# Performance work log

Hardware: AMD Instinct MI355X
Metric: run time of the kernel (lower is better)

## Reference

```python
import jax, jax.numpy as jnp
import numpy as np

D_MODEL = 1024
N_HEADS = 16
D_K = D_MODEL // N_HEADS
SEQ = 4096
BATCH = 1
THETA = 10000.0


def setup_inputs() -> dict:
    key = jax.random.key(0)
    ks = jax.random.split(key, 5)
    scale = 0.02
    x = jax.random.normal(ks[0], (BATCH, SEQ, D_MODEL), dtype=jnp.float32)
    token_positions = jnp.broadcast_to(jnp.arange(SEQ, dtype=jnp.int64 if jax.config.jax_enable_x64 else jnp.int32)[None, :], (BATCH, SEQ))
    Wq = jax.random.normal(ks[1], (D_MODEL, D_MODEL), dtype=jnp.float32) * scale
    Wk = jax.random.normal(ks[2], (D_MODEL, D_MODEL), dtype=jnp.float32) * scale
    Wv = jax.random.normal(ks[3], (D_MODEL, D_MODEL), dtype=jnp.float32) * scale
    Wo = jax.random.normal(ks[4], (D_MODEL, D_MODEL), dtype=jnp.float32) * scale
    return {"x": x, "token_positions": token_positions, "Wq": Wq, "Wk": Wk, "Wv": Wv, "Wo": Wo}


def _apply_rope(t, token_positions, theta=THETA):
    # t: (b, h, s, d_k); token_positions: (b, s)
    d_k = t.shape[-1]
    inv_freq = theta ** (-jnp.arange(0, d_k, 2, dtype=jnp.float32) / d_k)  # (d_k/2,)
    ang = token_positions.astype(jnp.float32)[:, :, None] * inv_freq  # (b, s, d_k/2)
    cos = jnp.cos(ang)[:, None, :, :]  # (b, 1, s, d_k/2)
    sin = jnp.sin(ang)[:, None, :, :]
    te, to = t[..., 0::2], t[..., 1::2]
    re = te * cos - to * sin
    ro = te * sin + to * cos
    # interleave back: (..., d_k/2, 2) -> (..., d_k)
    return jnp.stack([re, ro], axis=-1).reshape(t.shape)


def reference(x, token_positions, Wq, Wk, Wv, Wo):
    b, s, d_model = x.shape
    h, d_k = N_HEADS, D_K
    q = (x @ Wq.T).reshape(b, s, h, d_k).transpose(0, 2, 1, 3)  # (b,h,s,d_k)
    k = (x @ Wk.T).reshape(b, s, h, d_k).transpose(0, 2, 1, 3)
    v = (x @ Wv.T).reshape(b, s, h, d_k).transpose(0, 2, 1, 3)
    q = _apply_rope(q, token_positions)
    k = _apply_rope(k, token_positions)
    scores = jnp.einsum('bhqd,bhkd->bhqk', q, k) / jnp.sqrt(jnp.float32(d_k))
    causal = jnp.tril(jnp.ones((s, s), dtype=bool))[None, None]
    scores = jnp.where(causal, scores, jnp.float32(-1e9))
    attn = jax.nn.softmax(scores, axis=-1)
    out = jnp.einsum('bhqk,bhkd->bhqd', attn, v)  # (b,h,s,d_k)
    out = out.transpose(0, 2, 1, 3).reshape(b, s, d_model)
    return out @ Wo.T
```

## Files before the change

kernel.cpp:

```cpp
#include <hip/hip_runtime.h>
#include <hip/hip_bf16.h>
#include <math.h>


#define SEQ 4096
#define DM  1024
#define NH  16
#define DK  64

typedef __attribute__((ext_vector_type(8))) short short8;
typedef __attribute__((ext_vector_type(4))) float floatx4;
typedef __attribute__((ext_vector_type(16))) float floatx16;
typedef __attribute__((ext_vector_type(4))) short short4v;

static __device__ __forceinline__ short f2bf(float f) {
    __hip_bfloat16 h = __float2bfloat16(f);
    return __builtin_bit_cast(short, h);
}

static __device__ __forceinline__ float fast_exp2(float x) {
#if __has_builtin(__builtin_amdgcn_exp2f)
    return __builtin_amdgcn_exp2f(x);
#else
    return exp2f(x);
#endif
}

static __device__ __forceinline__ short8 load8_f32_as_bf16(const float* p) {
    float4 a = *reinterpret_cast<const float4*>(p);
    float4 b = *reinterpret_cast<const float4*>(p + 4);
    short8 s;
    s[0] = f2bf(a.x); s[1] = f2bf(a.y); s[2] = f2bf(a.z); s[3] = f2bf(a.w);
    s[4] = f2bf(b.x); s[5] = f2bf(b.y); s[6] = f2bf(b.z); s[7] = f2bf(b.w);
    return s;
}

static __device__ __forceinline__ void gl2lds16(const __hip_bfloat16* g, short* l) {
    __builtin_amdgcn_global_load_lds(
        (const __attribute__((address_space(1))) unsigned int*)g,
        (__attribute__((address_space(3))) unsigned int*)l, 16, 0, 0);
}

static __device__ __forceinline__ int read_pos(const int* tp32, int s) {
    return (tp32[1] == 1) ? tp32[s] : tp32[2 * s];
}

__global__ __launch_bounds__(256) void prep_kernel(
    const float* __restrict__ x,  const float* __restrict__ Wq,
    const float* __restrict__ Wk, const float* __restrict__ Wv,
    const int* __restrict__ tp,
    __hip_bfloat16* __restrict__ xb,  __hip_bfloat16* __restrict__ Wqb,
    __hip_bfloat16* __restrict__ Wkb, __hip_bfloat16* __restrict__ Wvb,
    float2* __restrict__ tab)
{
    int b = blockIdx.x;
    if (b < 3584) {
        const float* src; __hip_bfloat16* dst; int off;
        if (b < 2048)      { src = x;  dst = xb;  off = b; }
        else if (b < 2560) { src = Wq; dst = Wqb; off = b - 2048; }
        else if (b < 3072) { src = Wk; dst = Wkb; off = b - 2560; }
        else               { src = Wv; dst = Wvb; off = b - 3072; }
        size_t i = (size_t)off * 256 + threadIdx.x;
        short8 v = load8_f32_as_bf16(src + i * 8);
        *reinterpret_cast<short8*>((short*)dst + i * 8) = v;
    } else {
        int idx = (b - 3584) * 256 + threadIdx.x;
        if (idx < SEQ * 32) {
            int s = idx >> 5, pair = idx & 31;
            float inv_freq = exp2f(-(float)(2 * pair) * (13.287712379549449f / 64.f));
            float sn, cs;
            sincosf((float)read_pos(tp, s) * inv_freq, &sn, &cs);
            tab[idx] = make_float2(cs, sn);
        }
    }
}

__global__ __launch_bounds__(256) void qkv_rope_kernel(
    const __hip_bfloat16* __restrict__ xb,
    const float2* __restrict__ tab,
    const __hip_bfloat16* __restrict__ Wqb,
    const __hip_bfloat16* __restrict__ Wkb,
    const __hip_bfloat16* __restrict__ Wvb,
    __hip_bfloat16* __restrict__ q_ws,
    __hip_bfloat16* __restrict__ k_ws,
    __hip_bfloat16* __restrict__ vt_ws)
{
    __shared__ __align__(16) short pool[17408];
    short* As = pool;
    short* Bs = pool + 8192;

    const int by = blockIdx.y;
    const int wsel = by >> 3;
    const __hip_bfloat16* W = (wsel == 0) ? Wqb : (wsel == 1 ? Wkb : Wvb);
    const int nloc0 = (by & 7) * 128;
    const int m0 = blockIdx.x * 128;

    const int t = threadIdx.x;
    const int lane = t & 63;
    const int w = t >> 6;
    const int quad = lane >> 4;
    const int ln = lane & 15;
    const int wm = (w >> 1) * 64;
    const int wn = (w & 1) * 64;

    floatx4 acc[4][4];
    #pragma unroll
    for (int i = 0; i < 4; i++)
        #pragma unroll
        for (int j = 0; j < 4; j++) acc[i][j] = (floatx4){0.f, 0.f, 0.f, 0.f};

    for (int k0 = 0; k0 < DM; k0 += 64) {
        #pragma unroll
        for (int it = 0; it < 4; it++) {
            int row = w * 32 + it * 8 + (lane >> 3);
            int sg = (lane & 7) ^ (row & 7);
            gl2lds16(&xb[(size_t)(m0 + row) * DM + k0 + sg * 8], &As[(w * 32 + it * 8) * 64]);
            gl2lds16(&W[(size_t)(nloc0 + row) * DM + k0 + sg * 8], &Bs[(w * 32 + it * 8) * 64]);
        }
        __syncthreads();

        short8 af[4][2], bfr[4][2];
        #pragma unroll
        for (int i = 0; i < 4; i++)
            #pragma unroll
            for (int kc = 0; kc < 2; kc++)
                af[i][kc] = *reinterpret_cast<const short8*>(
                    &As[(wm + i * 16 + ln) * 64 + (((kc * 4 + quad) ^ (ln & 7)) << 3)]);
        #pragma unroll
        for (int j = 0; j < 4; j++)
            #pragma unroll
            for (int kc = 0; kc < 2; kc++)
                bfr[j][kc] = *reinterpret_cast<const short8*>(
                    &Bs[(wn + j * 16 + ln) * 64 + (((kc * 4 + quad) ^ (ln & 7)) << 3)]);

        #pragma unroll
        for (int kc = 0; kc < 2; kc++)
            #pragma unroll
            for (int i = 0; i < 4; i++)
                #pragma unroll
                for (int j = 0; j < 4; j++)
                    acc[i][j] = __builtin_amdgcn_mfma_f32_16x16x32_bf16(
                        af[i][kc], bfr[j][kc], acc[i][j], 0, 0, 0);
        __syncthreads();
    }

    if (wsel < 2) {
        __hip_bfloat16* dst = (wsel == 0) ? q_ws : k_ws;
        const float qscale = (wsel == 0) ? 0.18033688011112042f : 1.0f;
        #pragma unroll
        for (int j = 0; j < 4; j++) {
            int cnl = wn + j * 16 + ln;
            int pair = ((nloc0 + cnl) & 63) >> 1;
            #pragma unroll
            for (int i = 0; i < 4; i++) {
                int rowl = wm + i * 16 + quad * 4;
                #pragma unroll
                for (int r = 0; r < 4; r++) {
                    float2 t2 = tab[(size_t)(m0 + rowl + r) * 32 + pair];
                    float val = acc[i][j][r];
                    float partner = __shfl_xor(val, 1, 64);
                    float res = val * t2.x + (((lane & 1) ? partner : -partner) * t2.y);
                    pool[(rowl + r) * 136 + cnl] = f2bf(res * qscale);
                }
            }
        }
        __syncthreads();
        int row = t >> 1, half = t & 1;
        size_t gbase = (size_t)(m0 + row) * DM + nloc0 + half * 64;
        #pragma unroll
        for (int c = 0; c < 8; c++)
            *reinterpret_cast<short8*>(&dst[gbase + c * 8]) =
                *reinterpret_cast<const short8*>(&pool[row * 136 + half * 64 + c * 8]);
    } else {
        #pragma unroll
        for (int j = 0; j < 4; j++) {
            int cnl = wn + j * 16 + ln;
            #pragma unroll
            for (int i = 0; i < 4; i++) {
                int s0 = wm + i * 16 + quad * 4;
                #pragma unroll
                for (int r = 0; r < 4; r++)
                    pool[cnl * 136 + s0 + r] = f2bf(acc[i][j][r]);
            }
        }
        __syncthreads();
        int cnl = t >> 1, sh = t & 1;
        size_t base = (size_t)(nloc0 + cnl) * SEQ + m0 + sh * 64;
        #pragma unroll
        for (int c = 0; c < 8; c++)
            *reinterpret_cast<short8*>(&vt_ws[base + c * 8]) =
                *reinterpret_cast<const short8*>(&pool[cnl * 136 + sh * 64 + c * 8]);
    }
}

__global__ __launch_bounds__(1024, 1) void attn_kernel(
    const __hip_bfloat16* __restrict__ q_ws,
    const __hip_bfloat16* __restrict__ k_ws,
    const __hip_bfloat16* __restrict__ vt_ws,
    __hip_bfloat16* __restrict__ o_ws)
{
    __shared__ __align__(16) short Kt[2][128 * 64];
    __shared__ __align__(16) short Vt[2][64 * 128];

    const int bid = (int)blockIdx.x;
    const int head = bid & 15;
    const int jp = bid >> 4;

    const int t = threadIdx.x;
    const int lane = t & 63;
    const int w = t >> 6;
    const int ww = w & 3;
    const int kq = w >> 2;
    const int hi = lane >> 5;
    const int l31 = lane & 31;

    auto stage = [&](int b, int kb) {
        {
            int r = w * 8 + (lane >> 3);
            int keyloc = (r & ~12) | ((r & 4) << 1) | ((r & 8) >> 1);
            int g = (lane & 7) ^ (r & 7);
            gl2lds16(&k_ws[(size_t)(kb + keyloc) * DM + head * 64 + g * 8],
                     &Kt[b][(w * 8) * 64]);
        }
        {
            int d = w * 4 + (lane >> 4);
            int g = (lane & 15) ^ (d & 7);
            gl2lds16(&vt_ws[(size_t)(head * 64 + d) * SEQ + kb + g * 8],
                     &Vt[b][(w * 4) * 128]);
        }
    };

    #pragma unroll 1
    for (int pass = 0; pass < 2; pass++) {
        const int tile = pass ? jp : (31 - jp);
        const int nstep = tile + 1;
        const int q0 = tile * 128 + ww * 32;

        short8 qf[4];
        #pragma unroll
        for (int c = 0; c < 4; c++)
            qf[c] = *reinterpret_cast<const short8*>(
                &q_ws[(size_t)(q0 + l31) * DM + head * 64 + c * 16 + hi * 8]);

        floatx16 accO[2];
        #pragma unroll
        for (int db = 0; db < 2; db++)
            #pragma unroll
            for (int i = 0; i < 16; i++) accO[db][i] = 0.f;
        float l = 0.f;

        __syncthreads();
        stage(0, 0);
        int buf = 0;
        for (int st = 0; st < nstep; st++) {
            __syncthreads();
            if (st + 1 < nstep) stage(buf ^ 1, (st + 1) * 128);
            const bool last = (st == nstep - 1);

            if (!(last && kq > ww)) {
                const int kb32 = kq;
                const int krow = kb32 * 32 + l31;
                short8 kfr[4];
                #pragma unroll
                for (int kc = 0; kc < 4; kc++) {
                    int g = (kc * 2 + hi) ^ (krow & 7);
                    kfr[kc] = *reinterpret_cast<const short8*>(&Kt[buf][krow * 64 + g * 8]);
                }
                floatx16 s;
                #pragma unroll
                for (int i = 0; i < 16; i++) s[i] = 0.f;
                __builtin_amdgcn_s_setprio(1);
                #pragma unroll
                for (int kc = 0; kc < 4; kc++)
                    s = __builtin_amdgcn_mfma_f32_32x32x16_bf16(kfr[kc], qf[kc], s, 0, 0, 0);
                __builtin_amdgcn_s_setprio(0);

                if (last) {
                    #pragma unroll
                    for (int r = 0; r < 16; r++) {
                        int key_l = kb32 * 32 + (r & 7) + 2 * (r & 8) + 8 * hi;
                        if (key_l > ww * 32 + l31) s[r] = -1e9f;
                    }
                }
                float p[16];
                #pragma unroll
                for (int r = 0; r < 16; r++) { p[r] = fast_exp2(s[r]); l += p[r]; }

                union { short8 v; short e[8]; } pb[2];
                #pragma unroll
                for (int c = 0; c < 2; c++)
                    #pragma unroll
                    for (int e8 = 0; e8 < 8; e8++)
                        pb[c].e[e8] = f2bf(p[c * 8 + e8]);

                #pragma unroll
                for (int db = 0; db < 2; db++) {
                    const int vrow = db * 32 + l31;
                    short8 vfr[2];
                    #pragma unroll
                    for (int c = 0; c < 2; c++) {
                        int g = (kb32 * 4 + c * 2 + hi) ^ (vrow & 7);
                        vfr[c] = *reinterpret_cast<const short8*>(&Vt[buf][vrow * 128 + g * 8]);
                    }
                    __builtin_amdgcn_s_setprio(1);
                    accO[db] = __builtin_amdgcn_mfma_f32_32x32x16_bf16(vfr[0], pb[0].v, accO[db], 0, 0, 0);
                    accO[db] = __builtin_amdgcn_mfma_f32_32x32x16_bf16(vfr[1], pb[1].v, accO[db], 0, 0, 0);
                    __builtin_amdgcn_s_setprio(0);
                }
            }
            buf ^= 1;
        }

        float* scrK = (float*)Kt;
        float* scrV = (float*)Vt;
        __syncthreads();
        {
            const int slot = (ww * 2 + (kq & 1)) * 64 + lane;
            if (kq >= 2) {
                #pragma unroll
                for (int i = 0; i < 16; i++) scrK[i * 512 + slot] = accO[0][i];
                scrV[slot] = l;
            }
            __syncthreads();
            if (kq < 2) {
                #pragma unroll
                for (int i = 0; i < 16; i++) accO[0][i] += scrK[i * 512 + slot];
                l += scrV[slot];
            }
            __syncthreads();
            if (kq >= 2) {
                #pragma unroll
                for (int i = 0; i < 16; i++) scrK[i * 512 + slot] = accO[1][i];
            }
            __syncthreads();
            if (kq < 2) {
                #pragma unroll
                for (int i = 0; i < 16; i++) accO[1][i] += scrK[i * 512 + slot];
            }
            __syncthreads();
            const int slot2 = ww * 64 + lane;
            if (kq == 1) {
                #pragma unroll
                for (int i = 0; i < 16; i++) scrK[i * 256 + slot2] = accO[0][i];
                #pragma unroll
                for (int i = 0; i < 16; i++) scrK[(16 + i) * 256 + slot2] = accO[1][i];
                scrV[slot2] = l;
            }
            __syncthreads();
            if (kq == 0) {
                #pragma unroll
                for (int i = 0; i < 16; i++) accO[0][i] += scrK[i * 256 + slot2];
                #pragma unroll
                for (int i = 0; i < 16; i++) accO[1][i] += scrK[(16 + i) * 256 + slot2];
                l += scrV[slot2];
            }
        }

        float lf = l + __shfl_xor(l, 32, 64);
        float rl = 1.f / lf;

        __syncthreads();
        short* pool = (short*)Kt;
        if (kq == 0) {
            const int qrow = ww * 32 + l31;
            #pragma unroll
            for (int db = 0; db < 2; db++)
                #pragma unroll
                for (int j = 0; j < 4; j++) {
                    union { short4v v; short e[4]; } g;
                    #pragma unroll
                    for (int m = 0; m < 4; m++)
                        g.e[m] = f2bf(accO[db][j * 4 + m] * rl);
                    int dcol = db * 32 + j * 8 + 4 * hi;
                    *reinterpret_cast<short4v*>(&pool[qrow * 68 + dcol]) = g.v;
                }
        }
        __syncthreads();

        {
            int r = t >> 3, c8 = t & 7;
            size_t gb = (size_t)(tile * 128 + r) * DM + head * 64 + c8 * 8;
            union { short8 v8; short4v h[2]; } u;
            u.h[0] = *reinterpret_cast<const short4v*>(&pool[r * 68 + c8 * 8]);
            u.h[1] = *reinterpret_cast<const short4v*>(&pool[r * 68 + c8 * 8 + 4]);
            *reinterpret_cast<short8*>(&o_ws[gb]) = u.v8;
        }
    }
}

__global__ __launch_bounds__(256) void oproj_kernel(
    const __hip_bfloat16* __restrict__ o_in,
    const float* __restrict__ Wo,
    float* __restrict__ out)
{
    __shared__ __align__(16) char smem[24576];
    short* As = (short*)smem;
    short* Bs = As + 8192;
    float* fpool = (float*)smem;

    const int m0 = blockIdx.x * 128;
    const int n0 = blockIdx.y * 64;

    const int t = threadIdx.x;
    const int lane = t & 63;
    const int w = t >> 6;
    const int quad = lane >> 4;
    const int ln = lane & 15;
    const int wm = (w >> 1) * 64;
    const int wn = (w & 1) * 32;

    floatx4 acc[4][2];
    #pragma unroll
    for (int i = 0; i < 4; i++)
        #pragma unroll
        for (int j = 0; j < 2; j++) acc[i][j] = (floatx4){0.f, 0.f, 0.f, 0.f};

    for (int k0 = 0; k0 < DM; k0 += 64) {
        #pragma unroll
        for (int it = 0; it < 4; it++) {
            int row = w * 32 + it * 8 + (lane >> 3);
            int sg = (lane & 7) ^ (row & 7);
            gl2lds16(&o_in[(size_t)(m0 + row) * DM + k0 + sg * 8], &As[(w * 32 + it * 8) * 64]);
        }
        #pragma unroll
        for (int p = 0; p < 2; p++) {
            int r = (t >> 3) + p * 32;
            int sg2 = t & 7;
            *reinterpret_cast<short8*>(&Bs[r * 64 + ((sg2 ^ (r & 7)) << 3)]) =
                load8_f32_as_bf16(&Wo[(size_t)(n0 + r) * DM + k0 + sg2 * 8]);
        }
        __syncthreads();

        short8 af[4][2], bfr[2][2];
        #pragma unroll
        for (int i = 0; i < 4; i++)
            #pragma unroll
            for (int kc = 0; kc < 2; kc++)
                af[i][kc] = *reinterpret_cast<const short8*>(
                    &As[(wm + i * 16 + ln) * 64 + (((kc * 4 + quad) ^ (ln & 7)) << 3)]);
        #pragma unroll
        for (int j = 0; j < 2; j++)
            #pragma unroll
            for (int kc = 0; kc < 2; kc++)
                bfr[j][kc] = *reinterpret_cast<const short8*>(
                    &Bs[(wn + j * 16 + ln) * 64 + (((kc * 4 + quad) ^ (ln & 7)) << 3)]);

        #pragma unroll
        for (int kc = 0; kc < 2; kc++)
            #pragma unroll
            for (int i = 0; i < 4; i++)
                #pragma unroll
                for (int j = 0; j < 2; j++)
                    acc[i][j] = __builtin_amdgcn_mfma_f32_16x16x32_bf16(
                        af[i][kc], bfr[j][kc], acc[i][j], 0, 0, 0);
        __syncthreads();
    }

    #pragma unroll
    for (int ph = 0; ph < 2; ph++) {
        if ((w >> 1) == ph) {
            #pragma unroll
            for (int j = 0; j < 2; j++)
                #pragma unroll
                for (int i = 0; i < 4; i++) {
                    int rl = i * 16 + quad * 4;
                    #pragma unroll
                    for (int r = 0; r < 4; r++)
                        fpool[(rl + r) * 68 + wn + j * 16 + ln] = acc[i][j][r];
                }
        }
        __syncthreads();
        int row = t >> 2;
        int c0 = (t & 3) * 16;
        size_t gbase = (size_t)(m0 + ph * 64 + row) * DM + n0 + c0;
        #pragma unroll
        for (int c = 0; c < 4; c++)
            *reinterpret_cast<float4*>(&out[gbase + c * 4]) =
                *reinterpret_cast<const float4*>(&fpool[row * 68 + c0 + c * 4]);
        __syncthreads();
    }
}

extern "C" void kernel_launch(void* const* d_in, const int* in_sizes, int n_in,
                              void* d_out, int out_size, void* d_ws, size_t ws_size,
                              hipStream_t stream) {
    const float* x  = (const float*)d_in[0];
    const int* tp   = (const int*)d_in[1];
    const float* Wq = (const float*)d_in[2];
    const float* Wk = (const float*)d_in[3];
    const float* Wv = (const float*)d_in[4];
    const float* Wo = (const float*)d_in[5];
    float* out = (float*)d_out;

    char* ws = (char*)d_ws;
    const size_t MB = 1024 * 1024;
    __hip_bfloat16* xb    = (__hip_bfloat16*)(ws);
    __hip_bfloat16* q_ws  = (__hip_bfloat16*)(ws + 8  * MB);
    __hip_bfloat16* k_ws  = (__hip_bfloat16*)(ws + 16 * MB);
    __hip_bfloat16* vt_ws = (__hip_bfloat16*)(ws + 24 * MB);
    __hip_bfloat16* o_ws  = xb;
    __hip_bfloat16* Wqb = (__hip_bfloat16*)d_out;
    __hip_bfloat16* Wkb = Wqb + (size_t)DM * DM;
    __hip_bfloat16* Wvb = Wkb + (size_t)DM * DM;
    float2* tab = (float2*)((char*)d_out + 6 * MB);

    prep_kernel<<<4096, 256, 0, stream>>>(x, Wq, Wk, Wv, tp, xb, Wqb, Wkb, Wvb, tab);
    qkv_rope_kernel<<<dim3(32, 24), 256, 0, stream>>>(xb, tab, Wqb, Wkb, Wvb, q_ws, k_ws, vt_ws);
    attn_kernel<<<256, 1024, 0, stream>>>(q_ws, k_ws, vt_ws, o_ws);
    oproj_kernel<<<dim3(32, 16), 256, 0, stream>>>(o_ws, Wo, out);
}
```

Measured before the change: 205.0 us.

## Software-pipeline PV matmul one step behind QK in attention loop

Restructures the attention inner loop so the P·V MFMAs for the previous key tile run while the current tile's QK^T scores and exp are computed. V gains a third LDS buffer so the lagging tile stays resident, and a trailing P·V step is added after the loop. The setprio hints are dropped. The aim is to hide the softmax/exp latency behind matrix work and so remove the serial dependency between them. The cost is more LDS use and more live registers, which could hurt scheduling.

```diff
diff --git a/kernel.cpp b/kernel.cpp
--- a/kernel.cpp
+++ b/kernel.cpp
@@ -200,7 +200,7 @@
     __hip_bfloat16* __restrict__ o_ws)
 {
     __shared__ __align__(16) short Kt[2][128 * 64];
-    __shared__ __align__(16) short Vt[2][64 * 128];
+    __shared__ __align__(16) short Vt[3][64 * 128];
 
     const int bid = (int)blockIdx.x;
     const int head = bid & 15;
@@ -214,19 +214,19 @@
     const int hi = lane >> 5;
     const int l31 = lane & 31;
 
-    auto stage = [&](int b, int kb) {
+    auto stage = [&](int s, int kb) {
         {
             int r = w * 8 + (lane >> 3);
             int keyloc = (r & ~12) | ((r & 4) << 1) | ((r & 8) >> 1);
             int g = (lane & 7) ^ (r & 7);
             gl2lds16(&k_ws[(size_t)(kb + keyloc) * DM + head * 64 + g * 8],
-                     &Kt[b][(w * 8) * 64]);
+                     &Kt[s & 1][(w * 8) * 64]);
         }
         {
             int d = w * 4 + (lane >> 4);
             int g = (lane & 15) ^ (d & 7);
             gl2lds16(&vt_ws[(size_t)(head * 64 + d) * SEQ + kb + g * 8],
-                     &Vt[b][(w * 4) * 128]);
+                     &Vt[s % 3][(w * 4) * 128]);
         }
     };
 
@@ -248,37 +248,59 @@
             #pragma unroll
             for (int i = 0; i < 16; i++) accO[db][i] = 0.f;
         float l = 0.f;
+        short8 pbA, pbB;
 
         __syncthreads();
         stage(0, 0);
-        int buf = 0;
         for (int st = 0; st < nstep; st++) {
             __syncthreads();
-            if (st + 1 < nstep) stage(buf ^ 1, (st + 1) * 128);
+            if (st + 1 < nstep) stage(st + 1, (st + 1) * 128);
             const bool last = (st == nstep - 1);
-
-            if (!(last && kq > ww)) {
-                const int kb32 = kq;
-                const int krow = kb32 * 32 + l31;
-                short8 kfr[4];
+            const bool qk_act = !(last && kq > ww);
+
+            short8 kfr[4];
+            if (qk_act) {
+                const int krow = kq * 32 + l31;
                 #pragma unroll
                 for (int kc = 0; kc < 4; kc++) {
                     int g = (kc * 2 + hi) ^ (krow & 7);
-                    kfr[kc] = *reinterpret_cast<const short8*>(&Kt[buf][krow * 64 + g * 8]);
-                }
+                    kfr[kc] = *reinterpret_cast<const short8*>(&Kt[st & 1][krow * 64 + g * 8]);
+                }
+            }
+            short8 vfp[2][2];
+            if (st > 0) {
+                const short* Vp = Vt[(st - 1) % 3];
+                #pragma unroll
+                for (int db = 0; db < 2; db++) {
+                    const int vrow = db * 32 + l31;
+                    #pragma unroll
+                    for (int c = 0; c < 2; c++) {
+                        int g = (kq * 4 + c * 2 + hi) ^ (vrow & 7);
+                        vfp[db][c] = *reinterpret_cast<const short8*>(&Vp[vrow * 128 + g * 8]);
+                    }
+                }
+            }
+
+            if (st > 0) {
+                #pragma unroll
+                for (int db = 0; db < 2; db++) {
+                    accO[db] = __builtin_amdgcn_mfma_f32_32x32x16_bf16(vfp[db][0], pbA, accO[db], 0, 0, 0);
+                    accO[db] = __builtin_amdgcn_mfma_f32_32x32x16_bf16(vfp[db][1], pbB, accO[db], 0, 0, 0);
+                }
+            }
+
+            if (qk_act) {
                 floatx16 s;
                 #pragma unroll
                 for (int i = 0; i < 16; i++) s[i] = 0.f;
-                __builtin_amdgcn_s_setprio(1);
                 #pragma unroll
                 for (int kc = 0; kc < 4; kc++)
                     s = __builtin_amdgcn_mfma_f32_32x32x16_bf16(kfr[kc], qf[kc], s, 0, 0, 0);
-                __builtin_amdgcn_s_setprio(0);
 
                 if (last) {
                     #pragma unroll
                     for (int r = 0; r < 16; r++) {
-                        int key_l = kb32 * 32 + (r & 7) + 2 * (r & 8) + 8 * hi;
+                        int key_l = kq * 32 + (r & 7) + 2 * (r & 8) + 8 * hi;
                         if (key_l > ww * 32 + l31) s[r] = -1e9f;
                     }
                 }
@@ -286,29 +308,32 @@
                 #pragma unroll
                 for (int r = 0; r < 16; r++) { p[r] = fast_exp2(s[r]); l += p[r]; }
 
-                union { short8 v; short e[8]; } pb[2];
+                union { short8 v; short e[8]; } pk[2];
                 #pragma unroll
                 for (int c = 0; c < 2; c++)
                     #pragma unroll
                     for (int e8 = 0; e8 < 8; e8++)
-                        pb[c].e[e8] = f2bf(p[c * 8 + e8]);
-
-                #pragma unroll
-                for (int db = 0; db < 2; db++) {
-                    const int vrow = db * 32 + l31;
-                    short8 vfr[2];
-                    #pragma unroll
-                    for (int c = 0; c < 2; c++) {
-                        int g = (kb32 * 4 + c * 2 + hi) ^ (vrow & 7);
-                        vfr[c] = *reinterpret_cast<const short8*>(&Vt[buf][vrow * 128 + g * 8]);
-                    }
-                    __builtin_amdgcn_s_setprio(1);
-                    accO[db] = __builtin_amdgcn_mfma_f32_32x32x16_bf16(vfr[0], pb[0].v, accO[db], 0, 0, 0);
-                    accO[db] = __builtin_amdgcn_mfma_f32_32x32x16_bf16(vfr[1], pb[1].v, accO[db], 0, 0, 0);
-                    __builtin_amdgcn_s_setprio(0);
-                }
-            }
-            buf ^= 1;
+                        pk[c].e[e8] = f2bf(p[c * 8 + e8]);
+                pbA = pk[0].v;
+                pbB = pk[1].v;
+            }
+        }
+
+        if (!(kq > ww)) {
+            const short* Vp = Vt[(nstep - 1) % 3];
+            #pragma unroll
+            for (int db = 0; db < 2; db++) {
+                const int vrow = db * 32 + l31;
+                short8 vf0, vf1;
+                {
+                    int g = (kq * 4 + 0 * 2 + hi) ^ (vrow & 7);
+                    vf0 = *reinterpret_cast<const short8*>(&Vp[vrow * 128 + g * 8]);
+                    g = (kq * 4 + 1 * 2 + hi) ^ (vrow & 7);
+                    vf1 = *reinterpret_cast<const short8*>(&Vp[vrow * 128 + g * 8]);
+                }
+                accO[db] = __builtin_amdgcn_mfma_f32_32x32x16_bf16(vf0, pbA, accO[db], 0, 0, 0);
+                accO[db] = __builtin_amdgcn_mfma_f32_32x32x16_bf16(vf1, pbB, accO[db], 0, 0, 0);
+            }
         }
 
         float* scrK = (float*)Kt;
```

Measured after the change: 248.5 us. 21.2% more time.

## Software-pipeline PV matmul one step behind QK via LDS-staged probabilities

Applied to the files above, without the earlier changes.

The P·V MFMA for key tile st-1 now runs at the start of iteration st. Each wave writes its bf16 probabilities into a per-wave LDS slot and reads them back one step later. V staging moves to a triple buffer so the deferred V tile is still resident while the next tile is prefetched, and a final drain step handles the last tile. The aim is to overlap the exp/convert work of one tile with the matrix work of the previous tile. In exchange it adds an LDS write and read of P per step and raises shared memory use to about 112 KB.

```diff
diff --git a/kernel.cpp b/kernel.cpp
--- a/kernel.cpp
+++ b/kernel.cpp
@@ -200,7 +200,8 @@
     __hip_bfloat16* __restrict__ o_ws)
 {
     __shared__ __align__(16) short Kt[2][128 * 64];
-    __shared__ __align__(16) short Vt[2][64 * 128];
+    __shared__ __align__(16) short Vt[3][64 * 128];
+    __shared__ __align__(16) short Pl[16][1024];
 
     const int bid = (int)blockIdx.x;
     const int head = bid & 15;
@@ -214,20 +215,38 @@
     const int hi = lane >> 5;
     const int l31 = lane & 31;
 
-    auto stage = [&](int b, int kb) {
+    auto stage = [&](int s, int kb) {
         {
             int r = w * 8 + (lane >> 3);
             int keyloc = (r & ~12) | ((r & 4) << 1) | ((r & 8) >> 1);
             int g = (lane & 7) ^ (r & 7);
             gl2lds16(&k_ws[(size_t)(kb + keyloc) * DM + head * 64 + g * 8],
-                     &Kt[b][(w * 8) * 64]);
+                     &Kt[s & 1][(w * 8) * 64]);
         }
         {
             int d = w * 4 + (lane >> 4);
             int g = (lane & 15) ^ (d & 7);
             gl2lds16(&vt_ws[(size_t)(head * 64 + d) * SEQ + kb + g * 8],
-                     &Vt[b][(w * 4) * 128]);
-        }
+                     &Vt[s % 3][(w * 4) * 128]);
+        }
+    };
+
+    auto pv_step = [&](int s, floatx16* accO) {
+        const short* Vp = Vt[s % 3];
+        short8 pbA = *reinterpret_cast<const short8*>(&Pl[w][lane * 8]);
+        short8 pbB = *reinterpret_cast<const short8*>(&Pl[w][512 + lane * 8]);
+        __builtin_amdgcn_s_setprio(1);
+        #pragma unroll
+        for (int db = 0; db < 2; db++) {
+            const int vrow = db * 32 + l31;
+            int g0 = (kq * 4 + hi) ^ (vrow & 7);
+            int g1 = (kq * 4 + 2 + hi) ^ (vrow & 7);
+            short8 vf0 = *reinterpret_cast<const short8*>(&Vp[vrow * 128 + g0 * 8]);
+            short8 vf1 = *reinterpret_cast<const short8*>(&Vp[vrow * 128 + g1 * 8]);
+            accO[db] = __builtin_amdgcn_mfma_f32_32x32x16_bf16(vf0, pbA, accO[db], 0, 0, 0);
+            accO[db] = __builtin_amdgcn_mfma_f32_32x32x16_bf16(vf1, pbB, accO[db], 0, 0, 0);
+        }
+        __builtin_amdgcn_s_setprio(0);
     };
 
     #pragma unroll 1
@@ -251,20 +270,20 @@
 
         __syncthreads();
         stage(0, 0);
-        int buf = 0;
         for (int st = 0; st < nstep; st++) {
             __syncthreads();
-            if (st + 1 < nstep) stage(buf ^ 1, (st + 1) * 128);
+            if (st + 1 < nstep) stage(st + 1, (st + 1) * 128);
             const bool last = (st == nstep - 1);
 
+            if (st > 0) pv_step(st - 1, accO);
+
             if (!(last && kq > ww)) {
-                const int kb32 = kq;
-                const int krow = kb32 * 32 + l31;
+                const int krow = kq * 32 + l31;
                 short8 kfr[4];
                 #pragma unroll
                 for (int kc = 0; kc < 4; kc++) {
                     int g = (kc * 2 + hi) ^ (krow & 7);
-                    kfr[kc] = *reinterpret_cast<const short8*>(&Kt[buf][krow * 64 + g * 8]);
+                    kfr[kc] = *reinterpret_cast<const short8*>(&Kt[st & 1][krow * 64 + g * 8]);
                 }
                 floatx16 s;
                 #pragma unroll
@@ -278,7 +297,7 @@
                 if (last) {
                     #pragma unroll
                     for (int r = 0; r < 16; r++) {
-                        int key_l = kb32 * 32 + (r & 7) + 2 * (r & 8) + 8 * hi;
+                        int key_l = kq * 32 + (r & 7) + 2 * (r & 8) + 8 * hi;
                         if (key_l > ww * 32 + l31) s[r] = -1e9f;
                     }
                 }
@@ -286,30 +305,18 @@
                 #pragma unroll
                 for (int r = 0; r < 16; r++) { p[r] = fast_exp2(s[r]); l += p[r]; }
 
-                union { short8 v; short e[8]; } pb[2];
+                union { short8 v; short e[8]; } pk[2];
                 #pragma unroll
                 for (int c = 0; c < 2; c++)
                     #pragma unroll
                     for (int e8 = 0; e8 < 8; e8++)
-                        pb[c].e[e8] = f2bf(p[c * 8 + e8]);
-
-                #pragma unroll
-                for (int db = 0; db < 2; db++) {
-                    const int vrow = db * 32 + l31;
-                    short8 vfr[2];
-                    #pragma unroll
-                    for (int c = 0; c < 2; c++) {
-                        int g = (kb32 * 4 + c * 2 + hi) ^ (vrow & 7);
-                        vfr[c] = *reinterpret_cast<const short8*>(&Vt[buf][vrow * 128 + g * 8]);
-                    }
-                    __builtin_amdgcn_s_setprio(1);
-                    accO[db] = __builtin_amdgcn_mfma_f32_32x32x16_bf16(vfr[0], pb[0].v, accO[db], 0, 0, 0);
-                    accO[db] = __builtin_amdgcn_mfma_f32_32x32x16_bf16(vfr[1], pb[1].v, accO[db], 0, 0, 0);
-                    __builtin_amdgcn_s_setprio(0);
-                }
-            }
-            buf ^= 1;
-        }
+                        pk[c].e[e8] = f2bf(p[c * 8 + e8]);
+                *reinterpret_cast<short8*>(&Pl[w][lane * 8]) = pk[0].v;
+                *reinterpret_cast<short8*>(&Pl[w][512 + lane * 8]) = pk[1].v;
+            }
+        }
+
+        if (!(kq > ww)) pv_step(nstep - 1, accO);
 
         float* scrK = (float*)Kt;
         float* scrV = (float*)Vt;
```

Result: slower. 214.8 us (+4.8%).
